# Kernel optimization log

Measured on AMD Instinct MI355X. Metric: run time of the kernel, lower is better.

Reference implementation:

```python
import jax, jax.numpy as jnp
import numpy as np

SHAPES = [(100, 100), (50, 50), (25, 25), (13, 13)]
N_HEADS, N_LEVELS, N_POINTS, D_MODEL, D_FFN = 8, 4, 4, 256, 1024
HEAD_DIM = D_MODEL // N_HEADS
S_TOTAL = sum(h * w for h, w in SHAPES)
BATCH = 2


def _layernorm(x, g, b, eps=1e-5):
    m = jnp.mean(x, -1, keepdims=True)
    v = jnp.mean((x - m) ** 2, -1, keepdims=True)
    return (x - m) * jax.lax.rsqrt(v + eps) * g + b


def _bilinear_sample(value_l, loc, Hl, Wl):
    # value_l: (N, Hl, Wl, nh, hd); loc: (N, Lq, nh, P, 2) normalized to [0,1]
    # Matches torch grid_sample(mode='bilinear', padding_mode='zeros', align_corners=False)
    x = loc[..., 0] * Wl - 0.5
    y = loc[..., 1] * Hl - 0.5
    x0 = jnp.floor(x); y0 = jnp.floor(y)
    wx1 = x - x0; wx0 = 1.0 - wx1
    wy1 = y - y0; wy0 = 1.0 - wy1
    x0i = x0.astype(jnp.int32); x1i = x0i + 1
    y0i = y0.astype(jnp.int32); y1i = y0i + 1
    N, Lq, nh, P = x.shape
    n_idx = jnp.arange(N)[:, None, None, None]
    h_idx = jnp.arange(nh)[None, None, :, None]

    def gather(yi, xi):
        valid = (yi >= 0) & (yi < Hl) & (xi >= 0) & (xi < Wl)
        yc = jnp.clip(yi, 0, Hl - 1); xc = jnp.clip(xi, 0, Wl - 1)
        v = value_l[n_idx, yc, xc, h_idx]  # (N, Lq, nh, P, hd)
        return v * valid[..., None].astype(v.dtype)

    return (gather(y0i, x0i) * (wy0 * wx0)[..., None]
            + gather(y0i, x1i) * (wy0 * wx1)[..., None]
            + gather(y1i, x0i) * (wy1 * wx0)[..., None]
            + gather(y1i, x1i) * (wy1 * wx1)[..., None])


def _forward(src, pos, reference_points, W_off, b_off, W_attn, b_attn, W_val, b_val,
             W_out, b_out, W1, b1, W2, b2, g1, beta1, g2, beta2):
    N, S, C = src.shape
    q = src + pos  # with_pos_embed
    # MSDeformAttn
    off = (q @ W_off + b_off).reshape(N, S, N_HEADS, N_LEVELS, N_POINTS, 2)
    aw = jax.nn.softmax((q @ W_attn + b_attn).reshape(N, S, N_HEADS, N_LEVELS * N_POINTS), axis=-1)
    aw = aw.reshape(N, S, N_HEADS, N_LEVELS, N_POINTS)
    value = (src @ W_val + b_val).reshape(N, S, N_HEADS, HEAD_DIM)
    # offset normalizer is (W_l, H_l) per level
    normalizer = jnp.array([[wl, hl] for hl, wl in SHAPES], dtype=src.dtype)  # (L, 2)
    loc = reference_points[:, :, None, :, None, :] + off / normalizer[None, None, None, :, None, :]
    out = jnp.zeros((N, S, N_HEADS, HEAD_DIM), src.dtype)
    start = 0
    for l, (Hl, Wl) in enumerate(SHAPES):
        v_l = value[:, start:start + Hl * Wl].reshape(N, Hl, Wl, N_HEADS, HEAD_DIM)
        sampled = _bilinear_sample(v_l, loc[:, :, :, l], Hl, Wl)  # (N,S,nh,P,hd)
        out = out + jnp.einsum('nqhp,nqhpd->nqhd', aw[:, :, :, l], sampled)
        start += Hl * Wl
    src2 = out.reshape(N, S, C) @ W_out + b_out
    # residual + norm1 (dropout is identity in eval)
    x = _layernorm(src + src2, g1, beta1)
    # FFN + residual + norm2
    ff = jax.nn.relu(x @ W1 + b1) @ W2 + b2
    return _layernorm(x + ff, g2, beta2)


def setup_inputs() -> dict:
    key = jax.random.key(0)
    ks = jax.random.split(key, 16)
    f32 = jnp.float32

    def w(k, shape, scale=0.02):
        return jax.random.normal(k, shape, dtype=f32) * scale

    return {
        "src": jax.random.normal(ks[0], (BATCH, S_TOTAL, D_MODEL), dtype=f32),
        "pos": jax.random.normal(ks[1], (BATCH, S_TOTAL, D_MODEL), dtype=f32),
        "reference_points": jax.random.uniform(ks[2], (BATCH, S_TOTAL, N_LEVELS, 2), dtype=f32),
        "spatial_shapes": jnp.array(SHAPES, dtype=jnp.int32),
        "level_start_index": jnp.array(np.cumsum([0] + [h * w for h, w in SHAPES[:-1]]), dtype=jnp.int32),
        "W_off": w(ks[3], (D_MODEL, N_HEADS * N_LEVELS * N_POINTS * 2)),
        "b_off": w(ks[4], (N_HEADS * N_LEVELS * N_POINTS * 2,), 0.5),
        "W_attn": w(ks[5], (D_MODEL, N_HEADS * N_LEVELS * N_POINTS)),
        "b_attn": w(ks[6], (N_HEADS * N_LEVELS * N_POINTS,)),
        "W_val": w(ks[7], (D_MODEL, D_MODEL)),
        "b_val": w(ks[8], (D_MODEL,)),
        "W_out": w(ks[9], (D_MODEL, D_MODEL)),
        "b_out": w(ks[10], (D_MODEL,)),
        "W1": w(ks[11], (D_MODEL, D_FFN)),
        "b1": w(ks[12], (D_FFN,)),
        "W2": w(ks[13], (D_FFN, D_MODEL)),
        "b2": w(ks[14], (D_MODEL,)),
        "g1": jnp.ones((D_MODEL,), f32),
        "beta1": jnp.zeros((D_MODEL,), f32),
        "g2": jnp.ones((D_MODEL,), f32),
        "beta2": jnp.zeros((D_MODEL,), f32),
    }


def reference(src, pos, reference_points, spatial_shapes, level_start_index,
              W_off, b_off, W_attn, b_attn, W_val, b_val, W_out, b_out,
              W1, b1, W2, b2, g1, beta1, g2, beta2):
    # spatial_shapes / level_start_index are static metadata mirrored by SHAPES
    return _forward(src, pos, reference_points, W_off, b_off, W_attn, b_attn,
                    W_val, b_val, W_out, b_out, W1, b1, W2, b2, g1, beta1, g2, beta2)
```

## Files before the change

### kernel.cpp

```cpp
#include <hip/hip_runtime.h>


typedef __bf16 bf16x8 __attribute__((ext_vector_type(8)));
typedef __bf16 bf16x4 __attribute__((ext_vector_type(4)));
typedef float floatx4 __attribute__((ext_vector_type(4)));

#define S_TOTAL 13294
#define M_ROWS  26588
#define M_PAD   26624
#define DMODEL  256

#define GLDS(g, l)                                                            \
    __builtin_amdgcn_global_load_lds(                                         \
        (const __attribute__((address_space(1))) void*)(g),                   \
        (__attribute__((address_space(3))) void*)(l), 16, 0, 0)

__global__ __launch_bounds__(256) void convert_wt(const float* __restrict__ W,
                                                  __bf16* __restrict__ WT,
                                                  int K, int N) {
    int i = blockIdx.x * 256 + threadIdx.x;
    if (i >= N * K) return;
    int n = i / K, k = i - n * K;
    WT[i] = (__bf16)W[(size_t)k * N + n];
}

__global__ __launch_bounds__(256) void concat_bias(const float* __restrict__ b0,
                                                   const float* __restrict__ b1,
                                                   float* __restrict__ bc) {
    int i = blockIdx.x * 256 + threadIdx.x;
    if (i < 256) bc[i] = b0[i];
    else if (i < 384) bc[i] = b1[i - 256];
}

__global__ __launch_bounds__(256) void prep_k(const float* __restrict__ src,
                                              const float* __restrict__ pos,
                                              __bf16* __restrict__ qb,
                                              __bf16* __restrict__ srcb) {
    int i = blockIdx.x * 256 + threadIdx.x;
    if (i < M_ROWS * DMODEL) {
        float s = src[i];
        qb[i]   = (__bf16)(s + pos[i]);
        srcb[i] = (__bf16)s;
    } else {
        qb[i]   = (__bf16)0.f;
        srcb[i] = (__bf16)0.f;
    }
}

template <bool RELU, bool BF16OUT, bool ACCUM>
__global__ __launch_bounds__(256, 2) void gemm128(const __bf16* __restrict__ A,
                                                  const __bf16* __restrict__ BT,
                                                  const float* __restrict__ bias,
                                                  float* __restrict__ Cf,
                                                  __bf16* __restrict__ Cb,
                                                  int N, int K, int ldb) {
    __shared__ __align__(16) __bf16 As[128 * 32];
    __shared__ __align__(16) __bf16 Bs[128 * 32];
    const int tid  = threadIdx.x;
    const int bm   = blockIdx.y, bn = blockIdx.x;
    const int wave = tid >> 6, lane = tid & 63;
    const int wr   = wave >> 1, wc = wave & 1;
    const int l16  = lane & 15, quad = lane >> 4;

    floatx4 acc[4][4] = {};

    const int lr = tid >> 2;
    const int lc = (tid & 3) * 8;
    const __bf16* Ag0 = A  + (size_t)(bm * 128 + lr) * K + lc;
    const __bf16* Ag1 = Ag0 + (size_t)64 * K;
    const __bf16* Bg0 = BT + (size_t)(bn * 128 + lr) * ldb + lc;
    const __bf16* Bg1 = Bg0 + (size_t)64 * ldb;
    __bf16* Al0 = As + tid * 8;
    __bf16* Al1 = As + 64 * 32 + tid * 8;
    __bf16* Bl0 = Bs + tid * 8;
    __bf16* Bl1 = Bs + 64 * 32 + tid * 8;

    for (int k0 = 0; k0 < K; k0 += 32) {
        __syncthreads();
        GLDS(Ag0 + k0, Al0);
        GLDS(Ag1 + k0, Al1);
        GLDS(Bg0 + k0, Bl0);
        GLDS(Bg1 + k0, Bl1);
        __syncthreads();
        bf16x8 af[4], bf[4];
#pragma unroll
        for (int i = 0; i < 4; i++)
            af[i] = *(const bf16x8*)(As + (wr * 64 + i * 16 + l16) * 32 + quad * 8);
#pragma unroll
        for (int j = 0; j < 4; j++)
            bf[j] = *(const bf16x8*)(Bs + (wc * 64 + j * 16 + l16) * 32 + quad * 8);
#pragma unroll
        for (int i = 0; i < 4; i++)
#pragma unroll
            for (int j = 0; j < 4; j++)
                acc[i][j] = __builtin_amdgcn_mfma_f32_16x16x32_bf16(
                    af[i], bf[j], acc[i][j], 0, 0, 0);
    }

    const int row0 = bm * 128 + wr * 64;
    const int col0 = bn * 128 + wc * 64;
#pragma unroll
    for (int j = 0; j < 4; j++) {
        int   n  = col0 + j * 16 + l16;
        float bv = bias ? bias[n] : 0.f;
#pragma unroll
        for (int i = 0; i < 4; i++) {
            int m = row0 + i * 16 + quad * 4;
#pragma unroll
            for (int r = 0; r < 4; r++) {
                float v = acc[i][j][r] + bv;
                if (ACCUM) v += Cf[(size_t)(m + r) * N + n];
                if (RELU)  v = v > 0.f ? v : 0.f;
                if (BF16OUT) Cb[(size_t)(m + r) * N + n] = (__bf16)v;
                else         Cf[(size_t)(m + r) * N + n] = v;
            }
        }
    }
}

__global__ __launch_bounds__(256) void sample_k(const float* __restrict__ offa,
                                                const __bf16* __restrict__ valb,
                                                const float* __restrict__ refp,
                                                __bf16* __restrict__ outb) {
    const int r   = blockIdx.x;
    const int tid = threadIdx.x;
    if (r >= M_ROWS) {
        outb[(size_t)r * 256 + tid] = (__bf16)0.f;
        return;
    }
    __shared__ float s_log[128];
    __shared__ int   s_row[128][4];
    __shared__ float s_w[128][4];

    const int n = (r >= S_TOTAL) ? 1 : 0;

    if (tid < 128) s_log[tid] = offa[(size_t)r * 384 + 256 + tid];
    __syncthreads();

    if (tid < 128) {
        const int HL[4] = {100, 50, 25, 13};
        const int ST[4] = {0, 10000, 12500, 13125};
        int h = tid >> 4, lp = tid & 15, l = lp >> 2;
        float mx = -1e30f;
        for (int i = 0; i < 16; i++) mx = fmaxf(mx, s_log[h * 16 + i]);
        float sum = 0.f;
        for (int i = 0; i < 16; i++) sum += __expf(s_log[h * 16 + i] - mx);
        float aw = __expf(s_log[tid] - mx) / sum;

        float ox = offa[(size_t)r * 384 + tid * 2];
        float oy = offa[(size_t)r * 384 + tid * 2 + 1];
        float rx = refp[((size_t)r * 4 + l) * 2];
        float ry = refp[((size_t)r * 4 + l) * 2 + 1];
        int   Wl = HL[l], Hl = HL[l];
        float x = rx * (float)Wl + ox - 0.5f;
        float y = ry * (float)Hl + oy - 0.5f;
        float xf = floorf(x), yf = floorf(y);
        float wx1 = x - xf, wy1 = y - yf;
        float wx0 = 1.f - wx1, wy0 = 1.f - wy1;
        int x0 = (int)xf, y0 = (int)yf;
        int base = n * S_TOTAL + ST[l];
#pragma unroll
        for (int c = 0; c < 4; c++) {
            int yy = y0 + (c >> 1), xx = x0 + (c & 1);
            bool valid = (yy >= 0) & (yy < Hl) & (xx >= 0) & (xx < Wl);
            int yc = min(max(yy, 0), Hl - 1);
            int xc = min(max(xx, 0), Wl - 1);
            float w = ((c >> 1) ? wy1 : wy0) * ((c & 1) ? wx1 : wx0);
            s_row[tid][c] = base + yc * Wl + xc;
            s_w[tid][c]   = valid ? w * aw : 0.f;
        }
    }
    __syncthreads();

    const int h  = tid >> 5;
    const int pg = (tid >> 3) & 3;
    const int c4 = (tid & 7) * 4;
    const __bf16* vb = valb + h * 32 + c4;
    float a0 = 0.f, a1 = 0.f, a2 = 0.f, a3 = 0.f;
#pragma unroll
    for (int p = 0; p < 4; p++) {
        int idx = h * 16 + pg * 4 + p;
#pragma unroll
        for (int c = 0; c < 4; c++) {
            float w  = s_w[idx][c];
            int   rr = s_row[idx][c];
            bf16x4 v = *(const bf16x4*)(vb + (size_t)rr * 256);
            a0 += w * (float)v[0];
            a1 += w * (float)v[1];
            a2 += w * (float)v[2];
            a3 += w * (float)v[3];
        }
    }
    a0 += __shfl_xor(a0, 8);  a0 += __shfl_xor(a0, 16);
    a1 += __shfl_xor(a1, 8);  a1 += __shfl_xor(a1, 16);
    a2 += __shfl_xor(a2, 8);  a2 += __shfl_xor(a2, 16);
    a3 += __shfl_xor(a3, 8);  a3 += __shfl_xor(a3, 16);
    if (pg == 0) {
        bf16x4 res = {(__bf16)a0, (__bf16)a1, (__bf16)a2, (__bf16)a3};
        *(bf16x4*)(outb + (size_t)r * 256 + h * 32 + c4) = res;
    }
}

__global__ __launch_bounds__(64) void ln1_k(const float* __restrict__ src,
                                            const float* __restrict__ src2,
                                            const float* __restrict__ g,
                                            const float* __restrict__ b,
                                            float* __restrict__ x,
                                            __bf16* __restrict__ xb) {
    const int r = blockIdx.x, lane = threadIdx.x;
    if (r >= M_ROWS) {
        bf16x4 z = {(__bf16)0.f, (__bf16)0.f, (__bf16)0.f, (__bf16)0.f};
        *(bf16x4*)(xb + (size_t)r * 256 + lane * 4) = z;
        return;
    }
    size_t base = (size_t)r * 256 + lane * 4;
    float4 a = *(const float4*)(src + base);
    float4 c = *(const float4*)(src2 + base);
    float v0 = a.x + c.x, v1 = a.y + c.y, v2 = a.z + c.z, v3 = a.w + c.w;
    float s  = v0 + v1 + v2 + v3;
    float sq = v0 * v0 + v1 * v1 + v2 * v2 + v3 * v3;
    for (int o = 32; o > 0; o >>= 1) {
        s  += __shfl_xor(s, o);
        sq += __shfl_xor(sq, o);
    }
    float mean = s * (1.f / 256.f);
    float var  = sq * (1.f / 256.f) - mean * mean;
    float rs   = rsqrtf(var + 1e-5f);
    float4 gg = *(const float4*)(g + lane * 4);
    float4 bb = *(const float4*)(b + lane * 4);
    float o0 = (v0 - mean) * rs * gg.x + bb.x;
    float o1 = (v1 - mean) * rs * gg.y + bb.y;
    float o2 = (v2 - mean) * rs * gg.z + bb.z;
    float o3 = (v3 - mean) * rs * gg.w + bb.w;
    *(float4*)(x + base) = make_float4(o0, o1, o2, o3);
    bf16x4 ob = {(__bf16)o0, (__bf16)o1, (__bf16)o2, (__bf16)o3};
    *(bf16x4*)(xb + base) = ob;
}

__global__ __launch_bounds__(64) void ln2_k(const float* __restrict__ t,
                                            const float* __restrict__ g,
                                            const float* __restrict__ b,
                                            float* __restrict__ out) {
    const int r = blockIdx.x, lane = threadIdx.x;
    size_t base = (size_t)r * 256 + lane * 4;
    float4 a = *(const float4*)(t + base);
    float v0 = a.x, v1 = a.y, v2 = a.z, v3 = a.w;
    float s  = v0 + v1 + v2 + v3;
    float sq = v0 * v0 + v1 * v1 + v2 * v2 + v3 * v3;
    for (int o = 32; o > 0; o >>= 1) {
        s  += __shfl_xor(s, o);
        sq += __shfl_xor(sq, o);
    }
    float mean = s * (1.f / 256.f);
    float var  = sq * (1.f / 256.f) - mean * mean;
    float rs   = rsqrtf(var + 1e-5f);
    float4 gg = *(const float4*)(g + lane * 4);
    float4 bb = *(const float4*)(b + lane * 4);
    float4 o4;
    o4.x = (v0 - mean) * rs * gg.x + bb.x;
    o4.y = (v1 - mean) * rs * gg.y + bb.y;
    o4.z = (v2 - mean) * rs * gg.z + bb.z;
    o4.w = (v3 - mean) * rs * gg.w + bb.w;
    *(float4*)(out + base) = o4;
}

extern "C" void kernel_launch(void* const* d_in, const int* in_sizes, int n_in,
                              void* d_out, int out_size, void* d_ws, size_t ws_size,
                              hipStream_t stream) {
    const float* src  = (const float*)d_in[0];
    const float* pos  = (const float*)d_in[1];
    const float* refp = (const float*)d_in[2];
    const float* W_off  = (const float*)d_in[5];
    const float* b_off  = (const float*)d_in[6];
    const float* W_attn = (const float*)d_in[7];
    const float* b_attn = (const float*)d_in[8];
    const float* W_val  = (const float*)d_in[9];
    const float* b_val  = (const float*)d_in[10];
    const float* W_out  = (const float*)d_in[11];
    const float* b_out  = (const float*)d_in[12];
    const float* W1     = (const float*)d_in[13];
    const float* b1     = (const float*)d_in[14];
    const float* W2     = (const float*)d_in[15];
    const float* b2     = (const float*)d_in[16];
    const float* g1     = (const float*)d_in[17];
    const float* beta1  = (const float*)d_in[18];
    const float* g2     = (const float*)d_in[19];
    const float* beta2  = (const float*)d_in[20];
    float* out = (float*)d_out;

    const size_t RB = (size_t)M_PAD * 256 * 2;
    const size_t RF = (size_t)M_PAD * 256 * 4;
    char* ws = (char*)d_ws;
    __bf16* qb   = (__bf16*)(ws);
    __bf16* srcb = (__bf16*)(ws + RB);
    float*  offa = (float*)(ws + 2 * RB);
    __bf16* valb = (__bf16*)(ws + 2 * RB + (size_t)M_PAD * 384 * 4);
    __bf16* outb = qb;
    float*  src2 = (float*)(ws + RB);
    float*  x    = (float*)(ws + RB + RF);
    __bf16* xb   = qb;
    __bf16* hbh  = (__bf16*)(ws + 2 * RB + (size_t)M_PAD * 384 * 4);
    char*   regW = ws + 2 * RB + (size_t)M_PAD * 384 * 4 + (size_t)M_PAD * 512 * 2;

    __bf16* WTcomb = (__bf16*)regW;
    __bf16* WTval  = (__bf16*)(regW + 196608);
    __bf16* WTout  = (__bf16*)(regW + 327680);
    __bf16* WT1    = (__bf16*)(regW + 458752);
    __bf16* WT2    = (__bf16*)(regW + 983040);
    float*  bc     = (float*)(regW + 1507328);

    auto cvt = [&](const float* W, __bf16* WT, int K, int N) {
        convert_wt<<<(N * K + 255) / 256, 256, 0, stream>>>(W, WT, K, N);
    };
    cvt(W_off, WTcomb, 256, 256);
    cvt(W_attn, WTcomb + 65536, 256, 128);
    cvt(W_val, WTval, 256, 256);
    cvt(W_out, WTout, 256, 256);
    cvt(W1, WT1, 256, 1024);
    cvt(W2, WT2, 1024, 256);
    concat_bias<<<2, 256, 0, stream>>>(b_off, b_attn, bc);

    prep_k<<<M_PAD, 256, 0, stream>>>(src, pos, qb, srcb);

    gemm128<false, false, false><<<dim3(3, M_PAD / 128), 256, 0, stream>>>(
        qb, WTcomb, bc, offa, nullptr, 384, 256, 256);
    gemm128<false, true, false><<<dim3(2, M_PAD / 128), 256, 0, stream>>>(
        srcb, WTval, b_val, nullptr, valb, 256, 256, 256);

    sample_k<<<M_PAD, 256, 0, stream>>>(offa, valb, refp, outb);

    gemm128<false, false, false><<<dim3(2, M_PAD / 128), 256, 0, stream>>>(
        outb, WTout, b_out, src2, nullptr, 256, 256, 256);
    ln1_k<<<M_PAD, 64, 0, stream>>>(src, src2, g1, beta1, x, xb);

    for (int half = 0; half < 2; half++) {
        gemm128<true, true, false><<<dim3(4, M_PAD / 128), 256, 0, stream>>>(
            xb, WT1 + (size_t)half * 512 * 256, b1 + half * 512, nullptr, hbh,
            512, 256, 256);
        gemm128<false, false, true><<<dim3(2, M_PAD / 128), 256, 0, stream>>>(
            hbh, WT2 + half * 512, half == 0 ? b2 : nullptr, x, nullptr,
            256, 512, 1024);
    }
    ln2_k<<<M_ROWS, 64, 0, stream>>>(x, g2, beta2, out);
}
```

Before: 378.7 us.

## Fuse weight conversions, vectorize prep, stage GEMM epilogue via LDS, widen sampler loads

Merges the six weight-transpose launches and the bias concat into a single kernel. Vectorizes the prep kernel to float4 loads and bf16x4 stores. The GEMM epilogue now stages each wave's tile through LDS so global stores and the accumulate read-modify-write become row-contiguous float4 or bf16x4 accesses. The sampler computes softmax with wave shuffles instead of shared memory and packs weight and byte offset together in LDS. It also gathers 8 bf16 per load, which halves the point groups and adds an extra shuffle reduction step.

```diff
diff --git a/kernel.cpp b/kernel.cpp
--- a/kernel.cpp
+++ b/kernel.cpp
@@ -15,35 +15,53 @@
         (const __attribute__((address_space(1))) void*)(g),                   \
         (__attribute__((address_space(3))) void*)(l), 16, 0, 0)
 
-__global__ __launch_bounds__(256) void convert_wt(const float* __restrict__ W,
-                                                  __bf16* __restrict__ WT,
-                                                  int K, int N) {
+struct CvtArgs {
+    const float *Woff, *Wattn, *Wval, *Wout, *W1, *W2, *boff, *battn;
+};
+__global__ __launch_bounds__(256) void cvt_all(CvtArgs a, __bf16* __restrict__ wdst,
+                                               float* __restrict__ bc) {
     int i = blockIdx.x * 256 + threadIdx.x;
-    if (i >= N * K) return;
-    int n = i / K, k = i - n * K;
-    WT[i] = (__bf16)W[(size_t)k * N + n];
-}
-
-__global__ __launch_bounds__(256) void concat_bias(const float* __restrict__ b0,
-                                                   const float* __restrict__ b1,
-                                                   float* __restrict__ bc) {
-    int i = blockIdx.x * 256 + threadIdx.x;
-    if (i < 256) bc[i] = b0[i];
-    else if (i < 384) bc[i] = b1[i - 256];
+    if (i < 65536) {
+        wdst[i] = (__bf16)a.Woff[(i & 255) * 256 + (i >> 8)];
+    } else if (i < 98304) {
+        int j = i - 65536;
+        wdst[i] = (__bf16)a.Wattn[(j & 255) * 128 + (j >> 8)];
+    } else if (i < 163840) {
+        int j = i - 98304;
+        wdst[i] = (__bf16)a.Wval[(j & 255) * 256 + (j >> 8)];
+    } else if (i < 229376) {
+        int j = i - 163840;
+        wdst[i] = (__bf16)a.Wout[(j & 255) * 256 + (j >> 8)];
+    } else if (i < 491520) {
+        int j = i - 229376;
+        wdst[i] = (__bf16)a.W1[(j & 255) * 1024 + (j >> 8)];
+    } else if (i < 753664) {
+        int j = i - 491520;
+        wdst[i] = (__bf16)a.W2[(j & 1023) * 256 + (j >> 10)];
+    } else if (i < 754048) {
+        int j = i - 753664;
+        bc[j] = (j < 256) ? a.boff[j] : a.battn[j - 256];
+    }
 }
 
 __global__ __launch_bounds__(256) void prep_k(const float* __restrict__ src,
                                               const float* __restrict__ pos,
                                               __bf16* __restrict__ qb,
                                               __bf16* __restrict__ srcb) {
-    int i = blockIdx.x * 256 + threadIdx.x;
-    if (i < M_ROWS * DMODEL) {
-        float s = src[i];
-        qb[i]   = (__bf16)(s + pos[i]);
-        srcb[i] = (__bf16)s;
+    int i4 = blockIdx.x * 256 + threadIdx.x;
+    size_t e = (size_t)i4 * 4;
+    if (e < (size_t)M_ROWS * DMODEL) {
+        float4 s = *(const float4*)(src + e);
+        float4 p = *(const float4*)(pos + e);
+        bf16x4 q = {(__bf16)(s.x + p.x), (__bf16)(s.y + p.y),
+                    (__bf16)(s.z + p.z), (__bf16)(s.w + p.w)};
+        bf16x4 sb = {(__bf16)s.x, (__bf16)s.y, (__bf16)s.z, (__bf16)s.w};
+        *(bf16x4*)(qb + e)   = q;
+        *(bf16x4*)(srcb + e) = sb;
     } else {
-        qb[i]   = (__bf16)0.f;
-        srcb[i] = (__bf16)0.f;
+        bf16x4 z = {(__bf16)0.f, (__bf16)0.f, (__bf16)0.f, (__bf16)0.f};
+        *(bf16x4*)(qb + e)   = z;
+        *(bf16x4*)(srcb + e) = z;
     }
 }
 
@@ -54,8 +72,9 @@
                                                   float* __restrict__ Cf,
                                                   __bf16* __restrict__ Cb,
                                                   int N, int K, int ldb) {
-    __shared__ __align__(16) __bf16 As[128 * 32];
-    __shared__ __align__(16) __bf16 Bs[128 * 32];
+    __shared__ __align__(16) char smem[20480];
+    __bf16* As = (__bf16*)smem;
+    __bf16* Bs = (__bf16*)(smem + 8192);
     const int tid  = threadIdx.x;
     const int bm   = blockIdx.y, bn = blockIdx.x;
     const int wave = tid >> 6, lane = tid & 63;
@@ -82,37 +101,53 @@
         GLDS(Bg0 + k0, Bl0);
         GLDS(Bg1 + k0, Bl1);
         __syncthreads();
-        bf16x8 af[4], bf[4];
+        bf16x8 af[4], bfr[4];
 #pragma unroll
         for (int i = 0; i < 4; i++)
             af[i] = *(const bf16x8*)(As + (wr * 64 + i * 16 + l16) * 32 + quad * 8);
 #pragma unroll
         for (int j = 0; j < 4; j++)
-            bf[j] = *(const bf16x8*)(Bs + (wc * 64 + j * 16 + l16) * 32 + quad * 8);
+            bfr[j] = *(const bf16x8*)(Bs + (wc * 64 + j * 16 + l16) * 32 + quad * 8);
 #pragma unroll
         for (int i = 0; i < 4; i++)
 #pragma unroll
             for (int j = 0; j < 4; j++)
                 acc[i][j] = __builtin_amdgcn_mfma_f32_16x16x32_bf16(
-                    af[i], bf[j], acc[i][j], 0, 0, 0);
-    }
-
+                    af[i], bfr[j], acc[i][j], 0, 0, 0);
+    }
+
+    __syncthreads();
+    float* patch = (float*)smem + wave * (64 * 20);
     const int row0 = bm * 128 + wr * 64;
     const int col0 = bn * 128 + wc * 64;
+    const int plr = lane >> 2, plc = lane & 3;
+
 #pragma unroll
     for (int j = 0; j < 4; j++) {
         int   n  = col0 + j * 16 + l16;
         float bv = bias ? bias[n] : 0.f;
 #pragma unroll
-        for (int i = 0; i < 4; i++) {
-            int m = row0 + i * 16 + quad * 4;
+        for (int i = 0; i < 4; i++)
 #pragma unroll
             for (int r = 0; r < 4; r++) {
                 float v = acc[i][j][r] + bv;
-                if (ACCUM) v += Cf[(size_t)(m + r) * N + n];
-                if (RELU)  v = v > 0.f ? v : 0.f;
-                if (BF16OUT) Cb[(size_t)(m + r) * N + n] = (__bf16)v;
-                else         Cf[(size_t)(m + r) * N + n] = v;
+                if (RELU) v = fmaxf(v, 0.f);
+                patch[(i * 16 + quad * 4 + r) * 20 + l16] = v;
+            }
+#pragma unroll
+        for (int rr = 0; rr < 4; rr++) {
+            int row = rr * 16 + plr;
+            float4 v4 = *(float4*)&patch[row * 20 + plc * 4];
+            size_t gi = (size_t)(row0 + row) * N + col0 + j * 16 + plc * 4;
+            if (BF16OUT) {
+                bf16x4 ob = {(__bf16)v4.x, (__bf16)v4.y, (__bf16)v4.z, (__bf16)v4.w};
+                *(bf16x4*)(Cb + gi) = ob;
+            } else if (ACCUM) {
+                float4 c4 = *(const float4*)(Cf + gi);
+                v4.x += c4.x; v4.y += c4.y; v4.z += c4.z; v4.w += c4.w;
+                *(float4*)(Cf + gi) = v4;
+            } else {
+                *(float4*)(Cf + gi) = v4;
             }
         }
     }
@@ -128,76 +163,77 @@
         outb[(size_t)r * 256 + tid] = (__bf16)0.f;
         return;
     }
-    __shared__ float s_log[128];
-    __shared__ int   s_row[128][4];
-    __shared__ float s_w[128][4];
-
+    __shared__ float2 s_wo[128][4];
     const int n = (r >= S_TOTAL) ? 1 : 0;
 
-    if (tid < 128) s_log[tid] = offa[(size_t)r * 384 + 256 + tid];
-    __syncthreads();
-
     if (tid < 128) {
-        const int HL[4] = {100, 50, 25, 13};
-        const int ST[4] = {0, 10000, 12500, 13125};
-        int h = tid >> 4, lp = tid & 15, l = lp >> 2;
-        float mx = -1e30f;
-        for (int i = 0; i < 16; i++) mx = fmaxf(mx, s_log[h * 16 + i]);
-        float sum = 0.f;
-        for (int i = 0; i < 16; i++) sum += __expf(s_log[h * 16 + i] - mx);
-        float aw = __expf(s_log[tid] - mx) / sum;
-
-        float ox = offa[(size_t)r * 384 + tid * 2];
-        float oy = offa[(size_t)r * 384 + tid * 2 + 1];
+        const int HLc[4] = {100, 50, 25, 13};
+        const int STc[4] = {0, 10000, 12500, 13125};
+        int lp = tid & 15, l = lp >> 2;
+        float logit = offa[(size_t)r * 384 + 256 + tid];
+        float mx = logit;
+        mx = fmaxf(mx, __shfl_xor(mx, 1));
+        mx = fmaxf(mx, __shfl_xor(mx, 2));
+        mx = fmaxf(mx, __shfl_xor(mx, 4));
+        mx = fmaxf(mx, __shfl_xor(mx, 8));
+        float e = __expf(logit - mx);
+        float s = e;
+        s += __shfl_xor(s, 1); s += __shfl_xor(s, 2);
+        s += __shfl_xor(s, 4); s += __shfl_xor(s, 8);
+        float aw = e / s;
+
+        float2 o2 = *(const float2*)(offa + (size_t)r * 384 + tid * 2);
         float rx = refp[((size_t)r * 4 + l) * 2];
         float ry = refp[((size_t)r * 4 + l) * 2 + 1];
-        int   Wl = HL[l], Hl = HL[l];
-        float x = rx * (float)Wl + ox - 0.5f;
-        float y = ry * (float)Hl + oy - 0.5f;
+        int   Wl = HLc[l];
+        float x = rx * (float)Wl + o2.x - 0.5f;
+        float y = ry * (float)Wl + o2.y - 0.5f;
         float xf = floorf(x), yf = floorf(y);
         float wx1 = x - xf, wy1 = y - yf;
         float wx0 = 1.f - wx1, wy0 = 1.f - wy1;
         int x0 = (int)xf, y0 = (int)yf;
-        int base = n * S_TOTAL + ST[l];
+        int base = n * S_TOTAL + STc[l];
 #pragma unroll
         for (int c = 0; c < 4; c++) {
             int yy = y0 + (c >> 1), xx = x0 + (c & 1);
-            bool valid = (yy >= 0) & (yy < Hl) & (xx >= 0) & (xx < Wl);
-            int yc = min(max(yy, 0), Hl - 1);
+            bool valid = (yy >= 0) & (yy < Wl) & (xx >= 0) & (xx < Wl);
+            int yc = min(max(yy, 0), Wl - 1);
             int xc = min(max(xx, 0), Wl - 1);
             float w = ((c >> 1) ? wy1 : wy0) * ((c & 1) ? wx1 : wx0);
-            s_row[tid][c] = base + yc * Wl + xc;
-            s_w[tid][c]   = valid ? w * aw : 0.f;
+            int off = (base + yc * Wl + xc) * 512;
+            s_wo[tid][c] = make_float2(valid ? w * aw : 0.f, __int_as_float(off));
         }
     }
     __syncthreads();
 
     const int h  = tid >> 5;
-    const int pg = (tid >> 3) & 3;
-    const int c4 = (tid & 7) * 4;
-    const __bf16* vb = valb + h * 32 + c4;
-    float a0 = 0.f, a1 = 0.f, a2 = 0.f, a3 = 0.f;
-#pragma unroll
-    for (int p = 0; p < 4; p++) {
-        int idx = h * 16 + pg * 4 + p;
+    const int pg = (tid >> 2) & 7;
+    const int cg = tid & 3;
+    const char* vbase = (const char*)valb + h * 64 + cg * 16;
+    float a[8] = {};
+#pragma unroll
+    for (int pp = 0; pp < 2; pp++) {
+        int idx = h * 16 + pg * 2 + pp;
 #pragma unroll
         for (int c = 0; c < 4; c++) {
-            float w  = s_w[idx][c];
-            int   rr = s_row[idx][c];
-            bf16x4 v = *(const bf16x4*)(vb + (size_t)rr * 256);
-            a0 += w * (float)v[0];
-            a1 += w * (float)v[1];
-            a2 += w * (float)v[2];
-            a3 += w * (float)v[3];
+            float2 wo = s_wo[idx][c];
+            float  w  = wo.x;
+            bf16x8 v  = *(const bf16x8*)(vbase + __float_as_int(wo.y));
+#pragma unroll
+            for (int k = 0; k < 8; k++) a[k] += w * (float)v[k];
         }
     }
-    a0 += __shfl_xor(a0, 8);  a0 += __shfl_xor(a0, 16);
-    a1 += __shfl_xor(a1, 8);  a1 += __shfl_xor(a1, 16);
-    a2 += __shfl_xor(a2, 8);  a2 += __shfl_xor(a2, 16);
-    a3 += __shfl_xor(a3, 8);  a3 += __shfl_xor(a3, 16);
+#pragma unroll
+    for (int k = 0; k < 8; k++) {
+        a[k] += __shfl_xor(a[k], 4);
+        a[k] += __shfl_xor(a[k], 8);
+        a[k] += __shfl_xor(a[k], 16);
+    }
     if (pg == 0) {
-        bf16x4 res = {(__bf16)a0, (__bf16)a1, (__bf16)a2, (__bf16)a3};
-        *(bf16x4*)(outb + (size_t)r * 256 + h * 32 + c4) = res;
+        bf16x8 res;
+#pragma unroll
+        for (int k = 0; k < 8; k++) res[k] = (__bf16)a[k];
+        *(bf16x8*)(outb + (size_t)r * 256 + h * 32 + cg * 8) = res;
     }
 }
 
@@ -309,18 +345,10 @@
     __bf16* WT2    = (__bf16*)(regW + 983040);
     float*  bc     = (float*)(regW + 1507328);
 
-    auto cvt = [&](const float* W, __bf16* WT, int K, int N) {
-        convert_wt<<<(N * K + 255) / 256, 256, 0, stream>>>(W, WT, K, N);
-    };
-    cvt(W_off, WTcomb, 256, 256);
-    cvt(W_attn, WTcomb + 65536, 256, 128);
-    cvt(W_val, WTval, 256, 256);
-    cvt(W_out, WTout, 256, 256);
-    cvt(W1, WT1, 256, 1024);
-    cvt(W2, WT2, 1024, 256);
-    concat_bias<<<2, 256, 0, stream>>>(b_off, b_attn, bc);
-
-    prep_k<<<M_PAD, 256, 0, stream>>>(src, pos, qb, srcb);
+    CvtArgs ca = {W_off, W_attn, W_val, W_out, W1, W2, b_off, b_attn};
+    cvt_all<<<(754048 + 255) / 256, 256, 0, stream>>>(ca, WTcomb, bc);
+
+    prep_k<<<M_PAD * 256 / 4 / 256, 256, 0, stream>>>(src, pos, qb, srcb);
 
     gemm128<false, false, false><<<dim3(3, M_PAD / 128), 256, 0, stream>>>(
         qb, WTcomb, bc, offa, nullptr, 384, 256, 256);
```

After: 345.1 us. 1.1x faster.
